# Optimization experiments

Measured on AMD Instinct MI355X. Metric: run time of the kernel, lower is better.

The kernel has to match this reference:

```python
import jax, jax.numpy as jnp
import numpy as np

H = 16        # heads
DH = 64       # dim_head
DM = 1024     # query_dim = context_dim
INNER = H * DH


def setup_inputs() -> dict:
    key = jax.random.key(0)
    ks = jax.random.split(key, 5)
    s = 0.02
    queries = jax.random.normal(ks[0], (2, 2048, DM), dtype=jnp.float32)
    Wq = jax.random.normal(ks[1], (DM, INNER), dtype=jnp.float32) * s
    Wkv = jax.random.normal(ks[2], (DM, 2 * INNER), dtype=jnp.float32) * s
    Wo = jax.random.normal(ks[3], (INNER, DM), dtype=jnp.float32) * s
    bo = jax.random.normal(ks[4], (DM,), dtype=jnp.float32) * s
    return {"queries": queries, "Wq": Wq, "Wkv": Wkv, "Wo": Wo, "bo": bo}


def reference(queries, Wq, Wkv, Wo, bo):
    b, n, _ = queries.shape
    scale = DH ** -0.5
    q = queries @ Wq                       # [b, n, inner]
    kv = queries @ Wkv                     # self-attention: context = queries
    k, v = jnp.split(kv, 2, axis=-1)
    # b n (h d) -> b h n d
    split_heads = lambda t: t.reshape(b, n, H, DH).transpose(0, 2, 1, 3)
    q, k, v = map(split_heads, (q, k, v))
    sim = jnp.einsum('bhid,bhjd->bhij', q, k) * scale
    attn = jax.nn.softmax(sim, axis=-1)    # dropout is identity (p=0 / eval)
    out = jnp.einsum('bhij,bhjd->bhid', attn, v)
    out = out.transpose(0, 2, 1, 3).reshape(b, n, INNER)
    return out @ Wo + bo
```

## Files before the change

kernel.cpp:

```cpp
#include <hip/hip_runtime.h>
#include <math.h>
#include <stdint.h>

typedef _Float16 half8v __attribute__((ext_vector_type(8)));
typedef _Float16 half4v __attribute__((ext_vector_type(4)));
typedef float floatx4 __attribute__((ext_vector_type(4)));

#define MFMA16(a, b, c) __builtin_amdgcn_mfma_f32_16x16x32_f16(a, b, c, 0, 0, 0)
#define MFMA16K16(a, b, c) __builtin_amdgcn_mfma_f32_16x16x16f16(a, b, c, 0, 0, 0)

#define QSCALE 0.18033688011112f

__device__ __forceinline__ void gld_lds16(const void* g, void* l) {
  __builtin_amdgcn_global_load_lds(
      (const __attribute__((address_space(1))) uint32_t*)(uintptr_t)g,
      (__attribute__((address_space(3))) uint32_t*)(uintptr_t)l, 16, 0, 0);
}

__global__ __launch_bounds__(256) void convert_x(
    const float* __restrict__ X, _Float16* __restrict__ X16)
{
  size_t gid = (size_t)blockIdx.x * 256 + threadIdx.x;
  const float4* src = (const float4*)(X) + gid * 2;
  float4 a = src[0], b = src[1];
  half8v h;
  h[0]=(_Float16)a.x; h[1]=(_Float16)a.y; h[2]=(_Float16)a.z; h[3]=(_Float16)a.w;
  h[4]=(_Float16)b.x; h[5]=(_Float16)b.y; h[6]=(_Float16)b.z; h[7]=(_Float16)b.w;
  *((half8v*)X16 + gid) = h;
}

__global__ __launch_bounds__(256) void transpose_w(
    const float* __restrict__ Wq, const float* __restrict__ Wkv,
    const float* __restrict__ Wo,
    _Float16* __restrict__ WqkvT, _Float16* __restrict__ WoT)
{
  __shared__ alignas(16) _Float16 Tt[64 * 68];

  int b = blockIdx.x;
  const float* src; _Float16* dst; int N, tk, tn;
  if (b < 256)      { src = Wq;  dst = WqkvT;                 N = 1024; tk = b & 15;        tn = b >> 4; }
  else if (b < 768) { src = Wkv; dst = WqkvT + (size_t)1024 * 1024; N = 2048; tk = (b - 256) & 15; tn = (b - 256) >> 4; }
  else              { src = Wo;  dst = WoT;                   N = 1024; tk = (b - 768) & 15; tn = (b - 768) >> 4; }

  const int t = threadIdx.x;
  {
    int kg = t >> 4, ng = t & 15;
    const float* sp = src + (size_t)(tk * 64 + kg * 4) * N + tn * 64 + ng * 4;
    float4 r0 = *(const float4*)(sp);
    float4 r1 = *(const float4*)(sp + N);
    float4 r2 = *(const float4*)(sp + 2 * N);
    float4 r3 = *(const float4*)(sp + 3 * N);
    half4v h;
    h[0]=(_Float16)r0.x; h[1]=(_Float16)r1.x; h[2]=(_Float16)r2.x; h[3]=(_Float16)r3.x;
    *(half4v*)&Tt[(ng * 4 + 0) * 68 + kg * 4] = h;
    h[0]=(_Float16)r0.y; h[1]=(_Float16)r1.y; h[2]=(_Float16)r2.y; h[3]=(_Float16)r3.y;
    *(half4v*)&Tt[(ng * 4 + 1) * 68 + kg * 4] = h;
    h[0]=(_Float16)r0.z; h[1]=(_Float16)r1.z; h[2]=(_Float16)r2.z; h[3]=(_Float16)r3.z;
    *(half4v*)&Tt[(ng * 4 + 2) * 68 + kg * 4] = h;
    h[0]=(_Float16)r0.w; h[1]=(_Float16)r1.w; h[2]=(_Float16)r2.w; h[3]=(_Float16)r3.w;
    *(half4v*)&Tt[(ng * 4 + 3) * 68 + kg * 4] = h;
  }
  __syncthreads();
  #pragma unroll
  for (int i = 0; i < 2; i++) {
    int idx = t + i * 256;
    int nl = idx >> 3, k8 = (idx & 7) * 8;
    half8v v = *(half8v*)&Tt[nl * 68 + k8];
    *(half8v*)(dst + (size_t)(tn * 64 + nl) * 1024 + tk * 64 + k8) = v;
  }
}

__global__ __launch_bounds__(256) void qkv_gemm(
    const _Float16* __restrict__ X16, const _Float16* __restrict__ WqkvT,
    _Float16* __restrict__ q_ws, _Float16* __restrict__ k_ws,
    _Float16* __restrict__ vT_ws)
{
  constexpr int K = 1024;
  __shared__ alignas(16) _Float16 As[128 * 32];
  __shared__ alignas(16) _Float16 Bs[128 * 32];

  const int m0 = blockIdx.x * 128;
  const int n0 = blockIdx.y * 128;

  const int tid  = threadIdx.x;
  const int wave = tid >> 6, lane = tid & 63;
  const int qd = lane >> 4, l15 = lane & 15;
  const int wr = (wave >> 1) * 64, wc = (wave & 1) * 64;
  const int r0i = tid >> 2, c0 = (tid & 3) * 8;

  floatx4 acc[4][4] = {};

  for (int k0 = 0; k0 < K; k0 += 32) {
    gld_lds16(X16 + (size_t)(m0 + r0i) * K + k0 + c0, &As[tid * 8]);
    gld_lds16(X16 + (size_t)(m0 + 64 + r0i) * K + k0 + c0, &As[(tid + 256) * 8]);
    gld_lds16(WqkvT + (size_t)(n0 + r0i) * K + k0 + c0, &Bs[tid * 8]);
    gld_lds16(WqkvT + (size_t)(n0 + 64 + r0i) * K + k0 + c0, &Bs[(tid + 256) * 8]);
    __syncthreads();
    half8v a[4], b[4];
    #pragma unroll
    for (int it = 0; it < 4; it++)
      a[it] = *(half8v*)&As[(wr + it * 16 + l15) * 32 + qd * 8];
    #pragma unroll
    for (int jt = 0; jt < 4; jt++)
      b[jt] = *(half8v*)&Bs[(wc + jt * 16 + l15) * 32 + qd * 8];
    #pragma unroll
    for (int it = 0; it < 4; it++)
      #pragma unroll
      for (int jt = 0; jt < 4; jt++)
        acc[it][jt] = MFMA16(a[it], b[jt], acc[it][jt]);
    __syncthreads();
  }

  #pragma unroll
  for (int it = 0; it < 4; it++) {
    #pragma unroll
    for (int jt = 0; jt < 4; jt++) {
      #pragma unroll
      for (int r = 0; r < 4; r++) {
        int m = m0 + wr + it * 16 + qd * 4 + r;
        int n = n0 + wc + jt * 16 + l15;
        float val = acc[it][jt][r];
        int bb = m >> 11, nn = m & 2047;
        if (n0 < 1024) {
          int h = n >> 6, d = n & 63;
          q_ws[(((size_t)bb * 16 + h) * 2048 + nn) * 64 + d] = (_Float16)(val * QSCALE);
        } else if (n0 < 2048) {
          int c = n - 1024, h = c >> 6, d = c & 63;
          k_ws[(((size_t)bb * 16 + h) * 2048 + nn) * 64 + d] = (_Float16)val;
        } else {
          int c = n - 2048, h = c >> 6, d = c & 63;
          vT_ws[(((size_t)bb * 16 + h) * 64 + d) * 2048 + nn] = (_Float16)val;
        }
      }
    }
  }
}

__device__ __forceinline__ int swz(int row, int blk) {
  return row * 64 + ((blk ^ (row & 7)) << 3);
}

__global__ __launch_bounds__(128, 2) void attn_kernel(
    const _Float16* __restrict__ q_ws, const _Float16* __restrict__ k_ws,
    const _Float16* __restrict__ vT_ws, _Float16* __restrict__ aout)
{
  constexpr int N = 2048;
  __shared__ alignas(16) _Float16 Qs[64 * 64];
  __shared__ alignas(16) _Float16 Ks[64 * 64];
  __shared__ alignas(16) _Float16 Vts[64 * 64];

  const int id = blockIdx.x;
  const int bh = ((id >> 8) << 3) | (id & 7);
  const int qt = (id >> 3) & 31;

  const _Float16* Qp = q_ws + (size_t)bh * N * 64;
  const _Float16* Kp = k_ws + (size_t)bh * N * 64;
  const _Float16* Vp = vT_ws + (size_t)bh * 64 * N;

  const int tid = threadIdx.x, wave = tid >> 6, lane = tid & 63;
  const int qd = lane >> 4, l15 = lane & 15;
  const int q0 = qt * 64;
  const int wbase = wave * 32;

  #pragma unroll
  for (int i = 0; i < 4; i++) {
    int idx = tid + i * 128;
    int r = idx >> 3, blk = idx & 7;
    *(half8v*)&Qs[swz(r, blk)] =
        *(const half8v*)(Qp + (size_t)(q0 + r) * 64 + blk * 8);
  }
  __syncthreads();
  half8v qf[2][2];
  #pragma unroll
  for (int m = 0; m < 2; m++)
    #pragma unroll
    for (int ks = 0; ks < 2; ks++)
      qf[m][ks] = *(half8v*)&Qs[swz(wbase + m * 16 + l15, ks * 4 + qd)];

  floatx4 o[2][4] = {};
  float lsum[2] = {};

  half8v kpre[4], vpre[4];
  #pragma unroll
  for (int i = 0; i < 4; i++) {
    int idx = tid + i * 128;
    int r = idx >> 3, c8 = (idx & 7) * 8;
    kpre[i] = *(const half8v*)(Kp + (size_t)r * 64 + c8);
    vpre[i] = *(const half8v*)(Vp + (size_t)r * N + c8);
  }

  for (int kv0 = 0; kv0 < N; kv0 += 64) {
    __syncthreads();
    #pragma unroll
    for (int i = 0; i < 4; i++) {
      int idx = tid + i * 128;
      int r = idx >> 3, blk = idx & 7;
      *(half8v*)&Ks[swz(r, blk)]  = kpre[i];
      *(half8v*)&Vts[swz(r, blk)] = vpre[i];
    }
    if (kv0 + 64 < N) {
      int kvn = kv0 + 64;
      #pragma unroll
      for (int i = 0; i < 4; i++) {
        int idx = tid + i * 128;
        int r = idx >> 3, c8 = (idx & 7) * 8;
        kpre[i] = *(const half8v*)(Kp + (size_t)(kvn + r) * 64 + c8);
        vpre[i] = *(const half8v*)(Vp + (size_t)r * N + kvn + c8);
      }
    }
    __syncthreads();

    floatx4 s[4][2] = {};
    #pragma unroll
    for (int ks = 0; ks < 2; ks++) {
      half8v kf[4];
      #pragma unroll
      for (int nt = 0; nt < 4; nt++)
        kf[nt] = *(half8v*)&Ks[swz(nt * 16 + l15, ks * 4 + qd)];
      #pragma unroll
      for (int nt = 0; nt < 4; nt++)
        #pragma unroll
        for (int m = 0; m < 2; m++)
          s[nt][m] = MFMA16(kf[nt], qf[m][ks], s[nt][m]);
    }

    half4v pa[2][4];
    #pragma unroll
    for (int m = 0; m < 2; m++) {
      #pragma unroll
      for (int nt = 0; nt < 4; nt++) {
        #pragma unroll
        for (int r = 0; r < 4; r++) {
          float p = __builtin_amdgcn_exp2f(s[nt][m][r]);
          lsum[m] += p;
          pa[m][nt][r] = (_Float16)p;
        }
      }
    }

    #pragma unroll
    for (int ks2 = 0; ks2 < 4; ks2++) {
      half4v vf[4];
      #pragma unroll
      for (int dt = 0; dt < 4; dt++) {
        int row = dt * 16 + l15;
        int blk = 2 * ks2 + (qd >> 1);
        vf[dt] = *(half4v*)&Vts[row * 64 + ((blk ^ (row & 7)) << 3) + (qd & 1) * 4];
      }
      #pragma unroll
      for (int m = 0; m < 2; m++)
        #pragma unroll
        for (int dt = 0; dt < 4; dt++)
          o[m][dt] = MFMA16K16(pa[m][ks2], vf[dt], o[m][dt]);
    }
  }

  #pragma unroll
  for (int m = 0; m < 2; m++) {
    lsum[m] += __shfl_xor(lsum[m], 16);
    lsum[m] += __shfl_xor(lsum[m], 32);
  }

  const int bb = bh >> 4, hh = bh & 15;
  #pragma unroll
  for (int m = 0; m < 2; m++) {
    #pragma unroll
    for (int r = 0; r < 4; r++) {
      float inv = 1.0f / __shfl(lsum[m], qd * 4 + r);
      int n = q0 + wbase + m * 16 + qd * 4 + r;
      #pragma unroll
      for (int dt = 0; dt < 4; dt++) {
        int d = dt * 16 + l15;
        aout[((size_t)(bb * 2048 + n)) * 1024 + hh * 64 + d] =
            (_Float16)(o[m][dt][r] * inv);
      }
    }
  }
}

__global__ __launch_bounds__(256) void out_gemm(
    const _Float16* __restrict__ A, const _Float16* __restrict__ WoT,
    const float* __restrict__ bo, float* __restrict__ Out)
{
  constexpr int K = 1024;
  __shared__ alignas(16) _Float16 As[128 * 32];
  __shared__ alignas(16) _Float16 Bs[128 * 32];

  const int m0 = blockIdx.x * 128;
  const int n0 = blockIdx.y * 128;
  const int tid = threadIdx.x;
  const int wave = tid >> 6, lane = tid & 63;
  const int qd = lane >> 4, l15 = lane & 15;
  const int wr = (wave >> 1) * 64, wc = (wave & 1) * 64;
  const int r0i = tid >> 2, c0 = (tid & 3) * 8;

  floatx4 acc[4][4] = {};

  for (int k0 = 0; k0 < K; k0 += 32) {
    gld_lds16(A + (size_t)(m0 + r0i) * K + k0 + c0, &As[tid * 8]);
    gld_lds16(A + (size_t)(m0 + 64 + r0i) * K + k0 + c0, &As[(tid + 256) * 8]);
    gld_lds16(WoT + (size_t)(n0 + r0i) * K + k0 + c0, &Bs[tid * 8]);
    gld_lds16(WoT + (size_t)(n0 + 64 + r0i) * K + k0 + c0, &Bs[(tid + 256) * 8]);
    __syncthreads();
    half8v a[4], b[4];
    #pragma unroll
    for (int it = 0; it < 4; it++)
      a[it] = *(half8v*)&As[(wr + it * 16 + l15) * 32 + qd * 8];
    #pragma unroll
    for (int jt = 0; jt < 4; jt++)
      b[jt] = *(half8v*)&Bs[(wc + jt * 16 + l15) * 32 + qd * 8];
    #pragma unroll
    for (int it = 0; it < 4; it++)
      #pragma unroll
      for (int jt = 0; jt < 4; jt++)
        acc[it][jt] = MFMA16(a[it], b[jt], acc[it][jt]);
    __syncthreads();
  }

  #pragma unroll
  for (int it = 0; it < 4; it++) {
    #pragma unroll
    for (int jt = 0; jt < 4; jt++) {
      int n = n0 + wc + jt * 16 + l15;
      float bias = bo[n];
      #pragma unroll
      for (int r = 0; r < 4; r++) {
        int m = m0 + wr + it * 16 + qd * 4 + r;
        Out[(size_t)m * 1024 + n] = acc[it][jt][r] + bias;
      }
    }
  }
}

extern "C" void kernel_launch(void* const* d_in, const int* in_sizes, int n_in,
                              void* d_out, int out_size, void* d_ws, size_t ws_size,
                              hipStream_t stream) {
  const float* X   = (const float*)d_in[0];
  const float* Wq  = (const float*)d_in[1];
  const float* Wkv = (const float*)d_in[2];
  const float* Wo  = (const float*)d_in[3];
  const float* bo  = (const float*)d_in[4];
  float* out = (float*)d_out;

  const size_t M4 = (size_t)4 * 1024 * 1024;
  _Float16* q_ws   = (_Float16*)d_ws;
  _Float16* k_ws   = q_ws + M4;
  _Float16* vT_ws  = k_ws + M4;
  _Float16* X16    = vT_ws + M4;
  _Float16* WqkvT  = X16 + M4;
  _Float16* WoT    = WqkvT + (size_t)3 * 1024 * 1024;
  _Float16* aout   = X16;

  convert_x<<<2048, 256, 0, stream>>>(X, X16);
  transpose_w<<<1024, 256, 0, stream>>>(Wq, Wkv, Wo, WqkvT, WoT);
  qkv_gemm<<<dim3(32, 24), 256, 0, stream>>>(X16, WqkvT, q_ws, k_ws, vT_ws);
  attn_kernel<<<1024, 128, 0, stream>>>(q_ws, k_ws, vT_ws, aout);
  out_gemm<<<dim3(32, 8), 256, 0, stream>>>(aout, WoT, bo, out);
}
```

Baseline: 196.8 us.

## Double-buffer K/V tiles and route P through LDS for K32 MFMA

Makes the K and V shared-memory tiles double-buffered, so the next tile is stored into the spare buffer at the end of each iteration. This removes one of the two block barriers per KV step. The P·V product now stages the exponentiated scores, packed with round-toward-zero conversion, into the wave's own rows of the Q shared buffer. It then reads them back as 8-wide fragments so it can use the 16x16x32 MFMA instead of 16x16x16. In exchange it doubles K/V LDS usage, adds an LDS write and read of P per tile, and makes the fp16 conversion of P round toward zero.

New measurement: 197.8 us. Within noise of the previous version (+0.5%).

```diff
diff --git a/kernel.cpp b/kernel.cpp
--- a/kernel.cpp
+++ b/kernel.cpp
@@ -4,10 +4,11 @@
 
 typedef _Float16 half8v __attribute__((ext_vector_type(8)));
 typedef _Float16 half4v __attribute__((ext_vector_type(4)));
+typedef _Float16 half2v __attribute__((ext_vector_type(2)));
+typedef __fp16 fp16x2 __attribute__((ext_vector_type(2)));
 typedef float floatx4 __attribute__((ext_vector_type(4)));
 
 #define MFMA16(a, b, c) __builtin_amdgcn_mfma_f32_16x16x32_f16(a, b, c, 0, 0, 0)
-#define MFMA16K16(a, b, c) __builtin_amdgcn_mfma_f32_16x16x16f16(a, b, c, 0, 0, 0)
 
 #define QSCALE 0.18033688011112f
 
@@ -15,6 +16,11 @@
   __builtin_amdgcn_global_load_lds(
       (const __attribute__((address_space(1))) uint32_t*)(uintptr_t)g,
       (__attribute__((address_space(3))) uint32_t*)(uintptr_t)l, 16, 0, 0);
+}
+
+__device__ __forceinline__ half2v pk16(float a, float b) {
+  fp16x2 t = __builtin_amdgcn_cvt_pkrtz(a, b);
+  return __builtin_bit_cast(half2v, t);
 }
 
 __global__ __launch_bounds__(256) void convert_x(
@@ -146,8 +152,8 @@
 {
   constexpr int N = 2048;
   __shared__ alignas(16) _Float16 Qs[64 * 64];
-  __shared__ alignas(16) _Float16 Ks[64 * 64];
-  __shared__ alignas(16) _Float16 Vts[64 * 64];
+  __shared__ alignas(16) _Float16 Ks[2][64 * 64];
+  __shared__ alignas(16) _Float16 Vts[2][64 * 64];
 
   const int id = blockIdx.x;
   const int bh = ((id >> 8) << 3) | (id & 7);
@@ -188,17 +194,18 @@
     kpre[i] = *(const half8v*)(Kp + (size_t)r * 64 + c8);
     vpre[i] = *(const half8v*)(Vp + (size_t)r * N + c8);
   }
-
+  #pragma unroll
+  for (int i = 0; i < 4; i++) {
+    int idx = tid + i * 128;
+    int r = idx >> 3, blk = idx & 7;
+    *(half8v*)&Ks[0][swz(r, blk)]  = kpre[i];
+    *(half8v*)&Vts[0][swz(r, blk)] = vpre[i];
+  }
+
+  int p = 0;
   for (int kv0 = 0; kv0 < N; kv0 += 64) {
-    __syncthreads();
-    #pragma unroll
-    for (int i = 0; i < 4; i++) {
-      int idx = tid + i * 128;
-      int r = idx >> 3, blk = idx & 7;
-      *(half8v*)&Ks[swz(r, blk)]  = kpre[i];
-      *(half8v*)&Vts[swz(r, blk)] = vpre[i];
-    }
-    if (kv0 + 64 < N) {
+    const bool more = (kv0 + 64) < N;
+    if (more) {
       int kvn = kv0 + 64;
       #pragma unroll
       for (int i = 0; i < 4; i++) {
@@ -216,7 +223,7 @@
       half8v kf[4];
       #pragma unroll
       for (int nt = 0; nt < 4; nt++)
-        kf[nt] = *(half8v*)&Ks[swz(nt * 16 + l15, ks * 4 + qd)];
+        kf[nt] = *(half8v*)&Ks[p][swz(nt * 16 + l15, ks * 4 + qd)];
       #pragma unroll
       for (int nt = 0; nt < 4; nt++)
         #pragma unroll
@@ -224,35 +231,50 @@
           s[nt][m] = MFMA16(kf[nt], qf[m][ks], s[nt][m]);
     }
 
-    half4v pa[2][4];
     #pragma unroll
     for (int m = 0; m < 2; m++) {
       #pragma unroll
       for (int nt = 0; nt < 4; nt++) {
-        #pragma unroll
-        for (int r = 0; r < 4; r++) {
-          float p = __builtin_amdgcn_exp2f(s[nt][m][r]);
-          lsum[m] += p;
-          pa[m][nt][r] = (_Float16)p;
-        }
-      }
-    }
-
-    #pragma unroll
-    for (int ks2 = 0; ks2 < 4; ks2++) {
-      half4v vf[4];
-      #pragma unroll
-      for (int dt = 0; dt < 4; dt++) {
-        int row = dt * 16 + l15;
-        int blk = 2 * ks2 + (qd >> 1);
-        vf[dt] = *(half4v*)&Vts[row * 64 + ((blk ^ (row & 7)) << 3) + (qd & 1) * 4];
-      }
+        float p0 = __builtin_amdgcn_exp2f(s[nt][m][0]);
+        float p1 = __builtin_amdgcn_exp2f(s[nt][m][1]);
+        float p2 = __builtin_amdgcn_exp2f(s[nt][m][2]);
+        float p3 = __builtin_amdgcn_exp2f(s[nt][m][3]);
+        lsum[m] += (p0 + p1) + (p2 + p3);
+        half2v h01 = pk16(p0, p1);
+        half2v h23 = pk16(p2, p3);
+        half4v pk;
+        pk[0] = h01[0]; pk[1] = h01[1]; pk[2] = h23[0]; pk[3] = h23[1];
+        *(half4v*)&Qs[swz(wbase + m * 16 + l15, 2 * nt + (qd >> 1)) +
+                      (qd & 1) * 4] = pk;
+      }
+    }
+
+    #pragma unroll
+    for (int ks = 0; ks < 2; ks++) {
+      half8v pf[2], vf[4];
+      #pragma unroll
+      for (int m = 0; m < 2; m++)
+        pf[m] = *(half8v*)&Qs[swz(wbase + m * 16 + l15, 4 * ks + qd)];
+      #pragma unroll
+      for (int nt = 0; nt < 4; nt++)
+        vf[nt] = *(half8v*)&Vts[p][swz(nt * 16 + l15, 4 * ks + qd)];
       #pragma unroll
       for (int m = 0; m < 2; m++)
         #pragma unroll
-        for (int dt = 0; dt < 4; dt++)
-          o[m][dt] = MFMA16K16(pa[m][ks2], vf[dt], o[m][dt]);
-    }
+        for (int nt = 0; nt < 4; nt++)
+          o[m][nt] = MFMA16(pf[m], vf[nt], o[m][nt]);
+    }
+
+    if (more) {
+      #pragma unroll
+      for (int i = 0; i < 4; i++) {
+        int idx = tid + i * 128;
+        int r = idx >> 3, blk = idx & 7;
+        *(half8v*)&Ks[p ^ 1][swz(r, blk)]  = kpre[i];
+        *(half8v*)&Vts[p ^ 1][swz(r, blk)] = vpre[i];
+      }
+    }
+    p ^= 1;
   }
 
   #pragma unroll
```
